# Kernel tuning notes

Hardware: AMD Instinct MI355X
Metric: run time of the kernel (lower is better)

Reference implementation:

```python
import jax, jax.numpy as jnp
import numpy as np

B, S, C, H = 4, 2048, 256, 8  # batch, seq, hidden_dim (== per-head dim), n_heads


def setup_inputs() -> dict:
    key = jax.random.key(0)
    ks = jax.random.split(key, 9)
    sc_in = 1.0 / np.sqrt(C)
    sc_out = 1.0 / np.sqrt(C * H)
    return {
        "x":  jax.random.normal(ks[0], (B, S, C), dtype=jnp.float32),
        "Wq": jax.random.normal(ks[1], (C, C * H), dtype=jnp.float32) * sc_in,
        "bq": jax.random.normal(ks[2], (C * H,), dtype=jnp.float32) * 0.01,
        "Wk": jax.random.normal(ks[3], (C, C * H), dtype=jnp.float32) * sc_in,
        "bk": jax.random.normal(ks[4], (C * H,), dtype=jnp.float32) * 0.01,
        "Wv": jax.random.normal(ks[5], (C, C * H), dtype=jnp.float32) * sc_in,
        "bv": jax.random.normal(ks[6], (C * H,), dtype=jnp.float32) * 0.01,
        "Wo": jax.random.normal(ks[7], (C * H, C), dtype=jnp.float32) * sc_out,
        "bo": jax.random.normal(ks[8], (C,), dtype=jnp.float32) * 0.01,
    }


def reference(x, Wq, bq, Wk, bk, Wv, bv, Wo, bo):
    b, s, c = x.shape
    h = H
    # projections: (b, s, c) -> (b, s, h, c); per-head dim equals full hidden dim c
    q = (x @ Wq + bq).reshape(b, s, h, c)
    k = (x @ Wk + bk).reshape(b, s, h, c)
    v = (x @ Wv + bv).reshape(b, s, h, c)
    # scale q and k each by c**(-1/4) == total scale 1/sqrt(c)
    scale = jnp.asarray(c, x.dtype) ** -0.25
    q = q * scale
    k = k * scale
    # attention scores: (b, h, s_q, s_k)
    scores = jnp.einsum("bqhc,bkhc->bhqk", q, k)
    weights = jax.nn.softmax(scores, axis=-1)  # softmax over keys (torch dim=2 on (b*h, sq, sk))
    out = jnp.einsum("bhqk,bkhc->bqhc", weights, v).reshape(b, s, h * c)
    return out @ Wo + bo
```

## Files before the change

### kernel.cpp

```cpp
#include <hip/hip_runtime.h>
#include <stdint.h>
#include <math.h>

#define B_ 4
#define S_ 2048
#define C_ 256
#define H_ 8

typedef short bf16x8 __attribute__((ext_vector_type(8)));
typedef float f32x4 __attribute__((ext_vector_type(4)));
typedef float f32x16 __attribute__((ext_vector_type(16)));

static __device__ __forceinline__ short f2bf(float f) {
  uint32_t u = __float_as_uint(f);
  u = (u + 0x7fffu + ((u >> 16) & 1u)) >> 16;
  return (short)u;
}

static __device__ __forceinline__ int cvtpk(float lo, float hi) {
  int r;
  asm("v_cvt_pk_bf16_f32 %0, %1, %2" : "=v"(r) : "v"(lo), "v"(hi));
  return r;
}

static __device__ __forceinline__ bf16x8 pack4(int a, int b, int c, int d) {
  union { int i[4]; bf16x8 v; } u;
  u.i[0] = a; u.i[1] = b; u.i[2] = c; u.i[3] = d;
  return u.v;
}

static __device__ __forceinline__ void gld16(const void* g, void* l) {
  __builtin_amdgcn_global_load_lds(
      (const __attribute__((address_space(1))) uint32_t*)g,
      (__attribute__((address_space(3))) uint32_t*)l, 16, 0, 0);
}

__global__ void cvt_f32_bf16(const float* __restrict__ in, short* __restrict__ out, int n) {
  int i = (blockIdx.x * 256 + threadIdx.x) * 8;
  if (i >= n) return;
  float4 a = *(const float4*)(in + i);
  float4 b = *(const float4*)(in + i + 4);
  bf16x8 r;
  r[0] = f2bf(a.x); r[1] = f2bf(a.y); r[2] = f2bf(a.z); r[3] = f2bf(a.w);
  r[4] = f2bf(b.x); r[5] = f2bf(b.y); r[6] = f2bf(b.z); r[7] = f2bf(b.w);
  *(bf16x8*)(out + i) = r;
}

__global__ void transpose_cvt4(const float* __restrict__ Wq, const float* __restrict__ Wk,
                               const float* __restrict__ Wv, const float* __restrict__ Wo,
                               short* __restrict__ WqT, short* __restrict__ WkT,
                               short* __restrict__ WvT, short* __restrict__ WoT) {
  __shared__ float t[32][33];
  int bid = blockIdx.x;
  int which = bid >> 9, rem = bid & 511;
  const float* in; short* outp; int R, Cc, bx, by;
  if (which < 3) {
    R = 256; Cc = 2048; bx = rem & 63; by = rem >> 6;
    in = which == 0 ? Wq : (which == 1 ? Wk : Wv);
    outp = which == 0 ? WqT : (which == 1 ? WkT : WvT);
  } else {
    R = 2048; Cc = 256; bx = rem & 7; by = rem >> 3;
    in = Wo; outp = WoT;
  }
  int cb = bx * 32, rb = by * 32;
  int tr = threadIdx.x >> 5;
  int tc = threadIdx.x & 31;
#pragma unroll
  for (int i = 0; i < 4; i++)
    t[tr + i * 8][tc] = in[(size_t)(rb + tr + i * 8) * Cc + cb + tc];
  __syncthreads();
#pragma unroll
  for (int i = 0; i < 4; i++)
    outp[(size_t)(cb + tr + i * 8) * R + rb + tc] = f2bf(t[tc][tr + i * 8]);
}

template<int MODE>
__global__ void __launch_bounds__(256, 2) gemm_k(
    const short* __restrict__ A, const short* __restrict__ Bt,
    const float* __restrict__ bias, float scale, void* __restrict__ out,
    int M, int N, int K) {
  __shared__ char smem[36864];
  const int tid = threadIdx.x;
  const int l = tid & 63;
  const int w = tid >> 6;
  const int wr = w >> 1, wc = w & 1;
  const int mbase = blockIdx.y * 128;
  const int nbase = blockIdx.x * 128;

  const f32x4 fzero = {0.f, 0.f, 0.f, 0.f};
  f32x4 acc[4][4];
#pragma unroll
  for (int i = 0; i < 4; i++)
#pragma unroll
    for (int j = 0; j < 4; j++) acc[i][j] = fzero;

  const int kt0 = (MODE == 4) ? blockIdx.z * 16 : 0;
  const int nkt = (MODE == 4) ? 16 : (K >> 5);
  for (int kt = kt0; kt < kt0 + nkt; ++kt) {
#pragma unroll
    for (int c = 0; c < 2; c++) {
      int row = c * 64 + w * 16 + (l >> 2);
      const short* ga = A + (size_t)(mbase + row) * K + kt * 32 + (l & 3) * 8;
      gld16(ga, smem + (c * 4 + w) * 1024);
      const short* gb = Bt + (size_t)(nbase + row) * K + kt * 32 + (l & 3) * 8;
      gld16(gb, smem + 8192 + (c * 4 + w) * 1024);
    }
    __syncthreads();
    bf16x8 af[4], bf[4];
#pragma unroll
    for (int mf = 0; mf < 4; mf++)
      af[mf] = *(const bf16x8*)(smem + (wr * 64 + mf * 16 + (l & 15)) * 64 + ((l >> 4) << 4));
#pragma unroll
    for (int nf = 0; nf < 4; nf++)
      bf[nf] = *(const bf16x8*)(smem + 8192 + (wc * 64 + nf * 16 + (l & 15)) * 64 + ((l >> 4) << 4));
#pragma unroll
    for (int mf = 0; mf < 4; mf++)
#pragma unroll
      for (int nf = 0; nf < 4; nf++)
        acc[mf][nf] = __builtin_amdgcn_mfma_f32_16x16x32_bf16(af[mf], bf[nf], acc[mf][nf], 0, 0, 0);
    __syncthreads();
  }

  if (MODE == 0) {
#pragma unroll
    for (int mf = 0; mf < 4; mf++)
#pragma unroll
      for (int nf = 0; nf < 4; nf++)
#pragma unroll
        for (int i = 0; i < 4; i++) {
          int m = mbase + wr * 64 + mf * 16 + (l >> 4) * 4 + i;
          int n = nbase + wc * 64 + nf * 16 + (l & 15);
          float v = (acc[mf][nf][i] + bias[n]) * scale;
          int b = m >> 11, s = m & 2047;
          int h = n >> 8, d = n & 255;
          ((short*)out)[((size_t)(b * H_ + h) * S_ + s) * C_ + d] = f2bf(v);
        }
  } else if (MODE == 4) {
    float* pout = (float*)out + (size_t)blockIdx.z * M * N;
#pragma unroll
    for (int mf = 0; mf < 4; mf++)
#pragma unroll
      for (int nf = 0; nf < 4; nf++)
#pragma unroll
        for (int i = 0; i < 4; i++) {
          int m = mbase + wr * 64 + mf * 16 + (l >> 4) * 4 + i;
          int n = nbase + wc * 64 + nf * 16 + (l & 15);
          pout[(size_t)m * N + n] = acc[mf][nf][i];
        }
  } else {
    short* T = (short*)smem;
#pragma unroll
    for (int mf = 0; mf < 4; mf++)
#pragma unroll
      for (int nf = 0; nf < 4; nf++)
#pragma unroll
        for (int i = 0; i < 4; i++) {
          int ml = wr * 64 + mf * 16 + (l >> 4) * 4 + i;
          int nl = wc * 64 + nf * 16 + (l & 15);
          float v = (acc[mf][nf][i] + bias[nbase + nl]) * scale;
          T[ml * 136 + nl] = f2bf(v);
        }
    __syncthreads();
    int b = mbase >> 11, s0 = mbase & 2047;
    int h = nbase >> 8;
    int kt0e = s0 >> 5;
    char* hb = (char*)out + ((size_t)(b * H_ + h) << 20);
    if (MODE == 3) {
#pragma unroll
      for (int i2 = 0; i2 < 8; i2++) {
        int sid = tid * 8 + i2;
        int kt_l = sid >> 9, rem = sid & 511;
        int ksl = rem >> 6, lane2 = rem & 63;
        int tok = kt_l * 32 + (lane2 & 31);
        int dl = ksl * 16 + ((lane2 >> 5) << 3);
        bf16x8 v = *(const bf16x8*)&T[tok * 136 + dl];
        int ksg = ((nbase & 255) >> 4) + ksl;
        *(bf16x8*)(hb + ((size_t)(kt0e + kt_l) << 14) + ((ksg * 64 + lane2) << 4)) = v;
      }
    } else {
#pragma unroll
      for (int i2 = 0; i2 < 8; i2++) {
        int sid = tid * 8 + i2;
        int kt_l = sid >> 9, rem = sid & 511;
        int dtl = rem >> 7, kb = (rem >> 6) & 1, lane2 = rem & 63;
        int dl = dtl * 32 + (lane2 & 31);
        int k0 = kt_l * 32 + kb * 16 + ((lane2 >> 5) << 3);
        bf16x8 pk;
#pragma unroll
        for (int j = 0; j < 8; j++) pk[j] = T[(k0 + j) * 136 + dl];
        int dtg = ((nbase & 255) >> 5) + dtl;
        *(bf16x8*)(hb + ((size_t)(kt0e + kt_l) << 14) + (((dtg * 2 + kb) * 64 + lane2) << 4)) = pk;
      }
    }
  }
}

__global__ void reduce4(const float* __restrict__ part, const float* __restrict__ bias,
                        float* __restrict__ out) {
  const int MN = 8192 * 256;
  int i = (blockIdx.x * 256 + threadIdx.x) * 4;
  if (i >= MN) return;
  float4 a = *(const float4*)(part + i);
  float4 b = *(const float4*)(part + MN + i);
  float4 c = *(const float4*)(part + 2 * MN + i);
  float4 d = *(const float4*)(part + 3 * MN + i);
  float4 bs = *(const float4*)(bias + (i & 255));
  float4 r;
  r.x = a.x + b.x + c.x + d.x + bs.x;
  r.y = a.y + b.y + c.y + d.y + bs.y;
  r.z = a.z + b.z + c.z + d.z + bs.z;
  r.w = a.w + b.w + c.w + d.w + bs.w;
  *(float4*)(out + i) = r;
}

__global__ void __launch_bounds__(256, 2) attn_k(
    const short* __restrict__ Qg, const char* __restrict__ Kpk,
    const char* __restrict__ Vpk, short* __restrict__ Ag) {
  __shared__ char smem[65536];
  const int tid = threadIdx.x, l = tid & 63, w = tid >> 6;
  const int hi = l >> 5;
  const int lq = l & 31;

  if ((blockIdx.x >> 8) & 1) __builtin_amdgcn_s_sleep(42);

  const int orig = (blockIdx.x & 7) * 64 + (blockIdx.x >> 3);
  const int head = orig >> 4;
  const int qbase = (orig & 15) * 128 + w * 32;

  bf16x8 qf[16];
  {
    const short* qb = Qg + ((size_t)head * S_ + qbase + lq) * C_;
#pragma unroll
    for (int ks = 0; ks < 16; ks++) {
      qf[ks] = *(const bf16x8*)(qb + ks * 16 + hi * 8);
      asm volatile("" : "+v"(qf[ks]));
    }
  }

  f32x16 o[8];
#pragma unroll
  for (int dt = 0; dt < 8; dt++)
#pragma unroll
    for (int r = 0; r < 16; r++) o[dt][r] = 0.0f;
  float lrun = 0.0f;

  const char* kpH = Kpk + ((size_t)head << 20);
  const char* vpH = Vpk + ((size_t)head << 20);
  const int vo = tid << 4;
  const int lo = l << 4;

  auto STAGE = [&](int t) {
    char* Kd = smem + (t & 1) * 32768;
    char* Vd = Kd + 16384;
    const char* kq = kpH + ((size_t)t << 14);
    const char* vq = vpH + ((size_t)t << 14);
#pragma unroll
    for (int c = 0; c < 4; c++)
      gld16(kq + c * 4096 + vo, Kd + c * 4096 + vo);
#pragma unroll
    for (int c = 0; c < 4; c++)
      gld16(vq + c * 4096 + vo, Vd + c * 4096 + vo);
  };

  auto CALC = [&](int t) {
    const char* Ks = smem + (t & 1) * 32768;
    const char* Vs = Ks + 16384;
    f32x16 st;
#pragma unroll
    for (int r = 0; r < 16; r++) st[r] = 0.0f;
    __builtin_amdgcn_s_setprio(1);
#pragma unroll
    for (int ks = 0; ks < 16; ks++) {
      bf16x8 kf = *(const bf16x8*)(Ks + ks * 1024 + lo);
      st = __builtin_amdgcn_mfma_f32_32x32x16_bf16(kf, qf[ks], st, 0, 0, 0);
    }
    __builtin_amdgcn_s_setprio(0);
#pragma unroll
    for (int r = 0; r < 16; r++) st[r] = exp2f(st[r]);
    {
      float t0 = (st[0] + st[1]) + (st[2] + st[3]);
      float t1 = (st[4] + st[5]) + (st[6] + st[7]);
      float t2 = (st[8] + st[9]) + (st[10] + st[11]);
      float t3 = (st[12] + st[13]) + (st[14] + st[15]);
      lrun += (t0 + t1) + (t2 + t3);
    }
    __builtin_amdgcn_s_setprio(1);
    {
      int a0 = cvtpk(st[0], st[1]), a1 = cvtpk(st[2], st[3]);
      int a2 = cvtpk(st[4], st[5]), a3 = cvtpk(st[6], st[7]);
      auto s0p = __builtin_amdgcn_permlane32_swap(a0, a2, false, false);
      auto s1p = __builtin_amdgcn_permlane32_swap(a1, a3, false, false);
      bf16x8 pf0 = pack4(s0p[0], s1p[0], s0p[1], s1p[1]);
#pragma unroll
      for (int dt = 0; dt < 8; dt++) {
        bf16x8 v0 = *(const bf16x8*)(Vs + (dt * 2) * 1024 + lo);
        o[dt] = __builtin_amdgcn_mfma_f32_32x32x16_bf16(v0, pf0, o[dt], 0, 0, 0);
      }
    }
    {
      int a4 = cvtpk(st[8], st[9]),   a5 = cvtpk(st[10], st[11]);
      int a6 = cvtpk(st[12], st[13]), a7 = cvtpk(st[14], st[15]);
      auto s2p = __builtin_amdgcn_permlane32_swap(a4, a6, false, false);
      auto s3p = __builtin_amdgcn_permlane32_swap(a5, a7, false, false);
      bf16x8 pf1 = pack4(s2p[0], s3p[0], s2p[1], s3p[1]);
#pragma unroll
      for (int dt = 0; dt < 8; dt++) {
        bf16x8 v1 = *(const bf16x8*)(Vs + (dt * 2 + 1) * 1024 + lo);
        o[dt] = __builtin_amdgcn_mfma_f32_32x32x16_bf16(v1, pf1, o[dt], 0, 0, 0);
      }
    }
    __builtin_amdgcn_s_setprio(0);
  };

  STAGE(0);

#pragma unroll 1
  for (int t = 0; t < 64; ++t) {
    if (t < 63) {
      STAGE(t + 1);
      asm volatile("s_waitcnt vmcnt(8)" ::: "memory");
    } else {
      asm volatile("s_waitcnt vmcnt(0)" ::: "memory");
    }
    __builtin_amdgcn_s_barrier();
    CALC(t);
    asm volatile("" ::: "memory");
    __builtin_amdgcn_s_barrier();
  }

  float lsum = lrun + __shfl_xor(lrun, 32);
  float inv = 1.0f / lsum;
  char* ob = smem + w * 16384;
#pragma unroll
  for (int dt = 0; dt < 8; dt++) {
#pragma unroll
    for (int m = 0; m < 4; m++) {
      int lo32 = cvtpk(o[dt][4 * m + 0] * inv, o[dt][4 * m + 1] * inv);
      int hi32 = cvtpk(o[dt][4 * m + 2] * inv, o[dt][4 * m + 3] * inv);
      int cs = (dt * 4 + m) ^ lq;
      int* p = (int*)(ob + lq * 512 + cs * 16 + hi * 8);
      p[0] = lo32; p[1] = hi32;
    }
  }
  int bb = head >> 3, hh = head & 7;
#pragma unroll
  for (int pi = 0; pi < 16; pi++) {
    int qr = pi * 2 + hi;
    bf16x8 v = *(const bf16x8*)(ob + qr * 512 + ((lq ^ qr) << 4));
    size_t g = ((size_t)(bb * S_ + qbase + qr) * (H_ * C_)) + hh * C_ + lq * 8;
    *(bf16x8*)(Ag + g) = v;
  }
}

extern "C" void kernel_launch(void* const* d_in, const int* in_sizes, int n_in,
                              void* d_out, int out_size, void* d_ws, size_t ws_size,
                              hipStream_t stream) {
  const float* x  = (const float*)d_in[0];
  const float* Wq = (const float*)d_in[1];
  const float* bq = (const float*)d_in[2];
  const float* Wk = (const float*)d_in[3];
  const float* bk = (const float*)d_in[4];
  const float* Wv = (const float*)d_in[5];
  const float* bv = (const float*)d_in[6];
  const float* Wo = (const float*)d_in[7];
  const float* bo = (const float*)d_in[8];

  char* ws = (char*)d_ws;
  short* xb  = (short*)(ws);
  short* WqT = (short*)(ws + 4194304);
  short* WkT = (short*)(ws + 5242880);
  short* WvT = (short*)(ws + 6291456);
  short* WoT = (short*)(ws + 7340032);
  short* Qg  = (short*)(ws + 8388608);
  char*  Kpk = (char*)(ws + 41943040);
  char*  Vpk = (char*)(ws + 75497472);
  short* Ag  = (short*)(ws + 109051904);

  cvt_f32_bf16<<<1024, 256, 0, stream>>>(x, xb, 8192 * 256);
  transpose_cvt4<<<2048, 256, 0, stream>>>(Wq, Wk, Wv, Wo, WqT, WkT, WvT, WoT);

  const float scq = 0.25f * 1.44269504088896f;
  const float sck = 0.25f;
  gemm_k<0><<<dim3(16, 64), 256, 0, stream>>>(xb, WqT, bq, scq, Qg, 8192, 2048, 256);
  gemm_k<3><<<dim3(16, 64), 256, 0, stream>>>(xb, WkT, bk, sck, Kpk, 8192, 2048, 256);
  gemm_k<1><<<dim3(16, 64), 256, 0, stream>>>(xb, WvT, bv, 1.0f, Vpk, 8192, 2048, 256);
  attn_k<<<512, 256, 0, stream>>>(Qg, Kpk, Vpk, Ag);
  gemm_k<4><<<dim3(2, 64, 4), 256, 0, stream>>>(Ag, WoT, nullptr, 1.0f, Kpk, 8192, 256, 2048);
  reduce4<<<2048, 256, 0, stream>>>((const float*)Kpk, bo, (float*)d_out);
}
```

Measured before the change: 249.9 us.

## Merge prep kernels and QKV GEMMs into single launches; drop attention sleep/setprio

New measurement: 231.1 us. 7.5% less time.

```diff
diff --git a/kernel.cpp b/kernel.cpp
--- a/kernel.cpp
+++ b/kernel.cpp
@@ -35,24 +35,25 @@
       (__attribute__((address_space(3))) uint32_t*)l, 16, 0, 0);
 }
 
-__global__ void cvt_f32_bf16(const float* __restrict__ in, short* __restrict__ out, int n) {
-  int i = (blockIdx.x * 256 + threadIdx.x) * 8;
-  if (i >= n) return;
-  float4 a = *(const float4*)(in + i);
-  float4 b = *(const float4*)(in + i + 4);
-  bf16x8 r;
-  r[0] = f2bf(a.x); r[1] = f2bf(a.y); r[2] = f2bf(a.z); r[3] = f2bf(a.w);
-  r[4] = f2bf(b.x); r[5] = f2bf(b.y); r[6] = f2bf(b.z); r[7] = f2bf(b.w);
-  *(bf16x8*)(out + i) = r;
-}
-
-__global__ void transpose_cvt4(const float* __restrict__ Wq, const float* __restrict__ Wk,
-                               const float* __restrict__ Wv, const float* __restrict__ Wo,
-                               short* __restrict__ WqT, short* __restrict__ WkT,
-                               short* __restrict__ WvT, short* __restrict__ WoT) {
+__global__ void prep_k(const float* __restrict__ x, short* __restrict__ xb,
+                       const float* __restrict__ Wq, const float* __restrict__ Wk,
+                       const float* __restrict__ Wv, const float* __restrict__ Wo,
+                       short* __restrict__ WqT, short* __restrict__ WkT,
+                       short* __restrict__ WvT, short* __restrict__ WoT) {
+  int bid = blockIdx.x;
+  if (bid < 1024) {
+    int i = (bid * 256 + threadIdx.x) * 8;
+    float4 a = *(const float4*)(x + i);
+    float4 b = *(const float4*)(x + i + 4);
+    bf16x8 r;
+    r[0] = f2bf(a.x); r[1] = f2bf(a.y); r[2] = f2bf(a.z); r[3] = f2bf(a.w);
+    r[4] = f2bf(b.x); r[5] = f2bf(b.y); r[6] = f2bf(b.z); r[7] = f2bf(b.w);
+    *(bf16x8*)(xb + i) = r;
+    return;
+  }
   __shared__ float t[32][33];
-  int bid = blockIdx.x;
-  int which = bid >> 9, rem = bid & 511;
+  int tbid = bid - 1024;
+  int which = tbid >> 9, rem = tbid & 511;
   const float* in; short* outp; int R, Cc, bx, by;
   if (which < 3) {
     R = 256; Cc = 2048; bx = rem & 63; by = rem >> 6;
@@ -74,11 +75,13 @@
     outp[(size_t)(cb + tr + i * 8) * R + rb + tc] = f2bf(t[tc][tr + i * 8]);
 }
 
-template<int MODE>
-__global__ void __launch_bounds__(256, 2) gemm_k(
-    const short* __restrict__ A, const short* __restrict__ Bt,
-    const float* __restrict__ bias, float scale, void* __restrict__ out,
-    int M, int N, int K) {
+__global__ void __launch_bounds__(256, 2) gemm_qkv(
+    const short* __restrict__ A,
+    const short* __restrict__ WqT, const short* __restrict__ WkT,
+    const short* __restrict__ WvT,
+    const float* __restrict__ bq, const float* __restrict__ bk,
+    const float* __restrict__ bv,
+    short* __restrict__ Qg, char* __restrict__ Kpk, char* __restrict__ Vpk) {
   __shared__ char smem[36864];
   const int tid = threadIdx.x;
   const int l = tid & 63;
@@ -86,6 +89,11 @@
   const int wr = w >> 1, wc = w & 1;
   const int mbase = blockIdx.y * 128;
   const int nbase = blockIdx.x * 128;
+  const int z = blockIdx.z;
+
+  const short* Bt = z == 0 ? WqT : (z == 1 ? WkT : WvT);
+  const float* bias = z == 0 ? bq : (z == 1 ? bk : bv);
+  const float scale = z == 0 ? 0.25f * 1.44269504088896f : (z == 1 ? 0.25f : 1.0f);
 
   const f32x4 fzero = {0.f, 0.f, 0.f, 0.f};
   f32x4 acc[4][4];
@@ -94,15 +102,13 @@
 #pragma unroll
     for (int j = 0; j < 4; j++) acc[i][j] = fzero;
 
-  const int kt0 = (MODE == 4) ? blockIdx.z * 16 : 0;
-  const int nkt = (MODE == 4) ? 16 : (K >> 5);
-  for (int kt = kt0; kt < kt0 + nkt; ++kt) {
+  for (int kt = 0; kt < 8; ++kt) {
 #pragma unroll
     for (int c = 0; c < 2; c++) {
       int row = c * 64 + w * 16 + (l >> 2);
-      const short* ga = A + (size_t)(mbase + row) * K + kt * 32 + (l & 3) * 8;
+      const short* ga = A + (size_t)(mbase + row) * 256 + kt * 32 + (l & 3) * 8;
       gld16(ga, smem + (c * 4 + w) * 1024);
-      const short* gb = Bt + (size_t)(nbase + row) * K + kt * 32 + (l & 3) * 8;
+      const short* gb = Bt + (size_t)(nbase + row) * 256 + kt * 32 + (l & 3) * 8;
       gld16(gb, smem + 8192 + (c * 4 + w) * 1024);
     }
     __syncthreads();
@@ -121,7 +127,7 @@
     __syncthreads();
   }
 
-  if (MODE == 0) {
+  if (z == 0) {
 #pragma unroll
     for (int mf = 0; mf < 4; mf++)
 #pragma unroll
@@ -133,19 +139,7 @@
           float v = (acc[mf][nf][i] + bias[n]) * scale;
           int b = m >> 11, s = m & 2047;
           int h = n >> 8, d = n & 255;
-          ((short*)out)[((size_t)(b * H_ + h) * S_ + s) * C_ + d] = f2bf(v);
-        }
-  } else if (MODE == 4) {
-    float* pout = (float*)out + (size_t)blockIdx.z * M * N;
-#pragma unroll
-    for (int mf = 0; mf < 4; mf++)
-#pragma unroll
-      for (int nf = 0; nf < 4; nf++)
-#pragma unroll
-        for (int i = 0; i < 4; i++) {
-          int m = mbase + wr * 64 + mf * 16 + (l >> 4) * 4 + i;
-          int n = nbase + wc * 64 + nf * 16 + (l & 15);
-          pout[(size_t)m * N + n] = acc[mf][nf][i];
+          Qg[((size_t)(b * H_ + h) * S_ + s) * C_ + d] = f2bf(v);
         }
   } else {
     short* T = (short*)smem;
@@ -164,8 +158,8 @@
     int b = mbase >> 11, s0 = mbase & 2047;
     int h = nbase >> 8;
     int kt0e = s0 >> 5;
-    char* hb = (char*)out + ((size_t)(b * H_ + h) << 20);
-    if (MODE == 3) {
+    char* hb = (z == 1 ? Kpk : Vpk) + ((size_t)(b * H_ + h) << 20);
+    if (z == 1) {
 #pragma unroll
       for (int i2 = 0; i2 < 8; i2++) {
         int sid = tid * 8 + i2;
@@ -193,6 +187,63 @@
       }
     }
   }
+}
+
+__global__ void __launch_bounds__(256, 2) gemm_out(
+    const short* __restrict__ A, const short* __restrict__ Bt,
+    float* __restrict__ out, int M, int N, int K) {
+  __shared__ char smem[36864];
+  const int tid = threadIdx.x;
+  const int l = tid & 63;
+  const int w = tid >> 6;
+  const int wr = w >> 1, wc = w & 1;
+  const int mbase = blockIdx.y * 128;
+  const int nbase = blockIdx.x * 128;
+
+  const f32x4 fzero = {0.f, 0.f, 0.f, 0.f};
+  f32x4 acc[4][4];
+#pragma unroll
+  for (int i = 0; i < 4; i++)
+#pragma unroll
+    for (int j = 0; j < 4; j++) acc[i][j] = fzero;
+
+  const int kt0 = blockIdx.z * 16;
+  for (int kt = kt0; kt < kt0 + 16; ++kt) {
+#pragma unroll
+    for (int c = 0; c < 2; c++) {
+      int row = c * 64 + w * 16 + (l >> 2);
+      const short* ga = A + (size_t)(mbase + row) * K + kt * 32 + (l & 3) * 8;
+      gld16(ga, smem + (c * 4 + w) * 1024);
+      const short* gb = Bt + (size_t)(nbase + row) * K + kt * 32 + (l & 3) * 8;
+      gld16(gb, smem + 8192 + (c * 4 + w) * 1024);
+    }
+    __syncthreads();
+    bf16x8 af[4], bf[4];
+#pragma unroll
+    for (int mf = 0; mf < 4; mf++)
+      af[mf] = *(const bf16x8*)(smem + (wr * 64 + mf * 16 + (l & 15)) * 64 + ((l >> 4) << 4));
+#pragma unroll
+    for (int nf = 0; nf < 4; nf++)
+      bf[nf] = *(const bf16x8*)(smem + 8192 + (wc * 64 + nf * 16 + (l & 15)) * 64 + ((l >> 4) << 4));
+#pragma unroll
+    for (int mf = 0; mf < 4; mf++)
+#pragma unroll
+      for (int nf = 0; nf < 4; nf++)
+        acc[mf][nf] = __builtin_amdgcn_mfma_f32_16x16x32_bf16(af[mf], bf[nf], acc[mf][nf], 0, 0, 0);
+    __syncthreads();
+  }
+
+  float* pout = out + (size_t)blockIdx.z * M * N;
+#pragma unroll
+  for (int mf = 0; mf < 4; mf++)
+#pragma unroll
+    for (int nf = 0; nf < 4; nf++)
+#pragma unroll
+      for (int i = 0; i < 4; i++) {
+        int m = mbase + wr * 64 + mf * 16 + (l >> 4) * 4 + i;
+        int n = nbase + wc * 64 + nf * 16 + (l & 15);
+        pout[(size_t)m * N + n] = acc[mf][nf][i];
+      }
 }
 
 __global__ void reduce4(const float* __restrict__ part, const float* __restrict__ bias,
@@ -221,8 +272,6 @@
   const int hi = l >> 5;
   const int lq = l & 31;
 
-  if ((blockIdx.x >> 8) & 1) __builtin_amdgcn_s_sleep(42);
-
   const int orig = (blockIdx.x & 7) * 64 + (blockIdx.x >> 3);
   const int head = orig >> 4;
   const int qbase = (orig & 15) * 128 + w * 32;
@@ -268,13 +317,11 @@
     f32x16 st;
 #pragma unroll
     for (int r = 0; r < 16; r++) st[r] = 0.0f;
-    __builtin_amdgcn_s_setprio(1);
 #pragma unroll
     for (int ks = 0; ks < 16; ks++) {
       bf16x8 kf = *(const bf16x8*)(Ks + ks * 1024 + lo);
       st = __builtin_amdgcn_mfma_f32_32x32x16_bf16(kf, qf[ks], st, 0, 0, 0);
     }
-    __builtin_amdgcn_s_setprio(0);
 #pragma unroll
     for (int r = 0; r < 16; r++) st[r] = exp2f(st[r]);
     {
@@ -284,7 +331,6 @@
       float t3 = (st[12] + st[13]) + (st[14] + st[15]);
       lrun += (t0 + t1) + (t2 + t3);
     }
-    __builtin_amdgcn_s_setprio(1);
     {
       int a0 = cvtpk(st[0], st[1]), a1 = cvtpk(st[2], st[3]);
       int a2 = cvtpk(st[4], st[5]), a3 = cvtpk(st[6], st[7]);
@@ -309,7 +355,6 @@
         o[dt] = __builtin_amdgcn_mfma_f32_32x32x16_bf16(v1, pf1, o[dt], 0, 0, 0);
       }
     }
-    __builtin_amdgcn_s_setprio(0);
   };
 
   STAGE(0);
@@ -376,15 +421,10 @@
   char*  Vpk = (char*)(ws + 75497472);
   short* Ag  = (short*)(ws + 109051904);
 
-  cvt_f32_bf16<<<1024, 256, 0, stream>>>(x, xb, 8192 * 256);
-  transpose_cvt4<<<2048, 256, 0, stream>>>(Wq, Wk, Wv, Wo, WqT, WkT, WvT, WoT);
-
-  const float scq = 0.25f * 1.44269504088896f;
-  const float sck = 0.25f;
-  gemm_k<0><<<dim3(16, 64), 256, 0, stream>>>(xb, WqT, bq, scq, Qg, 8192, 2048, 256);
-  gemm_k<3><<<dim3(16, 64), 256, 0, stream>>>(xb, WkT, bk, sck, Kpk, 8192, 2048, 256);
-  gemm_k<1><<<dim3(16, 64), 256, 0, stream>>>(xb, WvT, bv, 1.0f, Vpk, 8192, 2048, 256);
+  prep_k<<<3072, 256, 0, stream>>>(x, xb, Wq, Wk, Wv, Wo, WqT, WkT, WvT, WoT);
+  gemm_qkv<<<dim3(16, 64, 3), 256, 0, stream>>>(xb, WqT, WkT, WvT, bq, bk, bv,
+                                                Qg, Kpk, Vpk);
   attn_k<<<512, 256, 0, stream>>>(Qg, Kpk, Vpk, Ag);
-  gemm_k<4><<<dim3(2, 64, 4), 256, 0, stream>>>(Ag, WoT, nullptr, 1.0f, Kpk, 8192, 256, 2048);
+  gemm_out<<<dim3(2, 64, 4), 256, 0, stream>>>(Ag, WoT, (float*)Kpk, 8192, 256, 2048);
   reduce4<<<2048, 256, 0, stream>>>((const float*)Kpk, bo, (float*)d_out);
 }
```
